# Kernel optimization log

Measured on AMD Instinct MI355X. Metric: run time of the kernel, lower is better.

Reference implementation:

```python
import jax, jax.numpy as jnp
import numpy as np

B, C, D = 1024, 100000, 512
S_SCALE, MARGIN, EPS = 64.0, 0.5, 1e-7  # arcface defaults


def setup_inputs() -> dict:
    key = jax.random.key(0)
    kx, kl, kw = jax.random.split(key, 3)
    x = jax.random.normal(kx, (B, D), dtype=jnp.float32)
    labels = jax.random.randint(kl, (B,), 0, C, dtype=jnp.int64)
    # nn.Linear default init: U(-1/sqrt(fan_in), 1/sqrt(fan_in))
    bound = 1.0 / np.sqrt(D)
    W = jax.random.uniform(kw, (C, D), dtype=jnp.float32, minval=-bound, maxval=bound)
    return {"x": x, "labels": labels, "W": W}


def reference(x, labels, W):
    # L2-normalize features (W is NOT normalized in the original -- the
    # normalize loop there rebinds a local and is a no-op).
    xn = x / jnp.maximum(jnp.linalg.norm(x, axis=1, keepdims=True), 1e-12)
    wf = jnp.einsum('bd,cd->bc', xn, W)               # [B, C] cosine-like logits
    target = jnp.take_along_axis(wf, labels[:, None], axis=1)[:, 0]  # [B]
    # arcface: s * cos(acos(clamp(cos_theta)) + m)
    numerator = S_SCALE * jnp.cos(
        jnp.arccos(jnp.clip(target, -1.0 + EPS, 1.0 - EPS)) + MARGIN)
    # sum over excluded classes = full sum - label term
    excl_sum = jnp.sum(jnp.exp(S_SCALE * wf), axis=1) - jnp.exp(S_SCALE * target)
    L = numerator - jnp.log(jnp.exp(numerator) + excl_sum)
    return -jnp.mean(L)
```

## Files before the change

### kernel.cpp

```cpp
#include <hip/hip_runtime.h>
#include <hip/hip_bf16.h>
#include <math.h>

#define NB 1024
#define NC 100000
#define ND 512
#define SSCALE 64.0f
#define MMARGIN 0.5f

#define BM 128
#define BN 128
#define BK 64
#define NKS (ND / BK)
#define NRT (NB / BM)
#define NCT ((NC + BN - 1) / BN)
#define GRIDSZ (NRT * NCT)

typedef __bf16 bf16x8 __attribute__((ext_vector_type(8)));
typedef float f32x4 __attribute__((ext_vector_type(4)));

__device__ __forceinline__ void gload_lds16(const void* g, void* l) {
    __builtin_amdgcn_global_load_lds(
        (const __attribute__((address_space(1))) unsigned int*)g,
        (__attribute__((address_space(3))) unsigned int*)l, 16, 0, 0);
}


__global__ void prep_kernel(const float* __restrict__ x, __bf16* __restrict__ xnb) {
    const int row = blockIdx.x;
    const int tid = threadIdx.x;
    const float2 v = *reinterpret_cast<const float2*>(x + (size_t)row * ND + tid * 2);
    float ss = v.x * v.x + v.y * v.y;
#pragma unroll
    for (int m = 1; m < 64; m <<= 1) ss += __shfl_xor(ss, m);
    __shared__ float wsum[4];
    if ((tid & 63) == 0) wsum[tid >> 6] = ss;
    __syncthreads();
    const float tot = wsum[0] + wsum[1] + wsum[2] + wsum[3];
    const float inv = 1.0f / fmaxf(sqrtf(tot), 1e-12f);
    __bf16* dst = xnb + (size_t)row * ND + tid * 2;
    dst[0] = (__bf16)(v.x * inv);
    dst[1] = (__bf16)(v.y * inv);
}

__global__ void target_kernel(const __bf16* __restrict__ xnb, const float* __restrict__ Wg,
                              const int* __restrict__ labels, float* __restrict__ tgt) {
    const int wid  = threadIdx.x >> 6;
    const int lane = threadIdx.x & 63;
    const int row  = blockIdx.x * 4 + wid;
    const int lab  = labels[row];
    const int k    = lane * 8;
    const bf16x8 xv = *reinterpret_cast<const bf16x8*>(xnb + (size_t)row * ND + k);
    const float* wr = Wg + (size_t)lab * ND + k;
    const float4 w0 = *reinterpret_cast<const float4*>(wr);
    const float4 w1 = *reinterpret_cast<const float4*>(wr + 4);
    float s = (float)xv[0] * w0.x + (float)xv[1] * w0.y + (float)xv[2] * w0.z + (float)xv[3] * w0.w
            + (float)xv[4] * w1.x + (float)xv[5] * w1.y + (float)xv[6] * w1.z + (float)xv[7] * w1.w;
#pragma unroll
    for (int m = 1; m < 64; m <<= 1) s += __shfl_xor(s, m);
    if (lane == 0) tgt[row] = s;
}

__global__ __launch_bounds__(256, 3) void gemm_exp_kernel(const __bf16* __restrict__ xnb,
                                                          const float* __restrict__ Wg,
                                                          float* __restrict__ sums) {
    __shared__ char lds[49152];
    const int tid  = threadIdx.x;
    const int wid  = tid >> 6;
    const int lane = tid & 63;
    const int l15  = lane & 15;
    const int lhi  = lane >> 4;
    const int wr   = wid >> 1;
    const int wc   = wid & 1;

    const int logical = (blockIdx.x & 7) * (GRIDSZ / 8) + (blockIdx.x >> 3);
    const int rt = logical & 7;
    const int ct = logical >> 3;
    const int r0 = rt * BM;
    const int c0 = ct * BN;

    float4 bw[8];

    const int bcls = (tid >> 3);
    const int bqp  = tid & 7;

    auto loadB = [&](int t) {
#pragma unroll
        for (int l = 0; l < 4; ++l) {
            const int cls = l * 32 + bcls;
            const float* src = Wg + (size_t)(c0 + cls) * ND + t * BK + bqp * 8;
            if (c0 + cls < NC) {
                bw[l * 2]     = *reinterpret_cast<const float4*>(src);
                bw[l * 2 + 1] = *reinterpret_cast<const float4*>(src + 4);
            } else {
                bw[l * 2]     = make_float4(0.f, 0.f, 0.f, 0.f);
                bw[l * 2 + 1] = make_float4(0.f, 0.f, 0.f, 0.f);
            }
        }
    };
    auto writeB = [&]() {
#pragma unroll
        for (int l = 0; l < 4; ++l) {
            const int cls = l * 32 + bcls;
            struct alignas(16) bf8s { __bf16 h[8]; };
            bf8s h;
            const float4 v0 = bw[l * 2], v1 = bw[l * 2 + 1];
            h.h[0] = (__bf16)v0.x; h.h[1] = (__bf16)v0.y; h.h[2] = (__bf16)v0.z; h.h[3] = (__bf16)v0.w;
            h.h[4] = (__bf16)v1.x; h.h[5] = (__bf16)v1.y; h.h[6] = (__bf16)v1.z; h.h[7] = (__bf16)v1.w;
            const int byte = 32768 + cls * 128 + ((bqp ^ (cls & 7)) << 4);
            *reinterpret_cast<bf8s*>(lds + byte) = h;
        }
    };
    auto stageA = [&](int t, int buf) {
#pragma unroll
        for (int it = 0; it < 4; ++it) {
            const int row = it * 32 + wid * 8 + (lane >> 3);
            const int c   = lane & 7;
            const int lc  = c ^ (row & 7);
            const char* src = (const char*)xnb + (size_t)(r0 + row) * (ND * 2) + t * (BK * 2) + lc * 16;
            char* dstbase = lds + buf * 16384 + it * 4096 + wid * 1024;
            gload_lds16(src, dstbase);
        }
    };

    f32x4 acc[4][4] = {};

    auto compute = [&](int buf) {
#pragma unroll
        for (int kk = 0; kk < 2; ++kk) {
            bf16x8 a[4], b[4];
#pragma unroll
            for (int i = 0; i < 4; ++i) {
                const int r = wr * 64 + i * 16 + l15;
                const int byte = buf * 16384 + r * 128 + ((((kk << 2) | lhi) ^ (r & 7)) << 4);
                a[i] = *reinterpret_cast<const bf16x8*>(lds + byte);
            }
#pragma unroll
            for (int j = 0; j < 4; ++j) {
                const int cc = wc * 64 + j * 16 + l15;
                const int byte = 32768 + cc * 128 + ((((kk << 2) | lhi) ^ (cc & 7)) << 4);
                b[j] = *reinterpret_cast<const bf16x8*>(lds + byte);
            }
#pragma unroll
            for (int i = 0; i < 4; ++i)
#pragma unroll
                for (int j = 0; j < 4; ++j)
                    acc[i][j] = __builtin_amdgcn_mfma_f32_16x16x32_bf16(a[i], b[j], acc[i][j], 0, 0, 0);
        }
    };

    loadB(0);
    stageA(0, 0);
    writeB();
    __syncthreads();
    int cur = 0;
#pragma unroll 1
    for (int t = 0; t < NKS; ++t) {
        if (t + 1 < NKS) {
            loadB(t + 1);
            stageA(t + 1, cur ^ 1);
        }
        compute(cur);
        __syncthreads();
        if (t + 1 < NKS) writeB();
        __syncthreads();
        cur ^= 1;
    }

#pragma unroll
    for (int i = 0; i < 4; ++i) {
#pragma unroll
        for (int r = 0; r < 4; ++r) {
            float v = 0.f;
#pragma unroll
            for (int j = 0; j < 4; ++j) {
                const int c = c0 + wc * 64 + j * 16 + l15;
                v += (c < NC) ? __expf(SSCALE * acc[i][j][r]) : 0.f;
            }
            v += __shfl_xor(v, 1);
            v += __shfl_xor(v, 2);
            v += __shfl_xor(v, 4);
            v += __shfl_xor(v, 8);
            if (l15 == 0) {
                const int row = r0 + wr * 64 + i * 16 + lhi * 4 + r;
                atomicAdd(&sums[row], v);
            }
        }
    }
}

__global__ void finalize_kernel(const float* __restrict__ sums, const float* __restrict__ tgt,
                                float* __restrict__ out) {
    const int tid  = threadIdx.x;
    const int wid  = tid >> 6;
    const int lane = tid & 63;
    float t  = tgt[tid];
    const float se = sums[tid];
    t = fminf(fmaxf(t, -1.0f + 1e-7f), 1.0f - 1e-7f);
    const float numer = SSCALE * cosf(acosf(t) + MMARGIN);
    const float excl  = se - expf(SSCALE * t);
    float L = numer - logf(expf(numer) + excl);
#pragma unroll
    for (int m = 1; m < 64; m <<= 1) L += __shfl_xor(L, m);
    __shared__ float ws2[16];
    if (lane == 0) ws2[wid] = L;
    __syncthreads();
    if (tid == 0) {
        float tot = 0.f;
        for (int i = 0; i < 16; ++i) tot += ws2[i];
        out[0] = -(tot / (float)NB);
    }
}

extern "C" void kernel_launch(void* const* d_in, const int* in_sizes, int n_in,
                              void* d_out, int out_size, void* d_ws, size_t ws_size,
                              hipStream_t stream) {
    const float* x      = (const float*)d_in[0];
    const int*   labels = (const int*)d_in[1];
    const float* W      = (const float*)d_in[2];
    float* out = (float*)d_out;

    char* wsb = (char*)d_ws;
    __bf16* xnb  = (__bf16*)wsb;
    float*  sums = (float*)(wsb + (size_t)NB * ND * 2);
    float*  tgt  = sums + NB;

    hipMemsetAsync(sums, 0, NB * sizeof(float), stream);
    prep_kernel<<<NB, 256, 0, stream>>>(x, xnb);
    target_kernel<<<NB / 4, 256, 0, stream>>>(xnb, W, labels, tgt);
    gemm_exp_kernel<<<GRIDSZ, 256, 0, stream>>>(xnb, W, sums);
    finalize_kernel<<<1, 1024, 0, stream>>>(sums, tgt, out);
}
```

Baseline: 194.1 us.

## Pre-convert W to bf16 and stage both GEMM operands via direct global-to-LDS loads

Adds a separate pass that converts W (fp32) to a padded bf16 copy in workspace. The GEMM then stages both A and B tiles with global_load_lds into double-buffered LDS, removing per-block fp32 loads, register conversion and the extra barrier. W is read once at fp32 and once at bf16 instead of being re-read in fp32 by all 8 row tiles. In exchange LDS grows to 64KB, occupancy drops to 2 blocks per CU, and the conversion pass plus workspace space are needed; the old register path remains as a fallback with double-buffered B.

```diff
diff --git a/kernel.cpp b/kernel.cpp
--- a/kernel.cpp
+++ b/kernel.cpp
@@ -15,6 +15,11 @@
 #define NRT (NB / BM)
 #define NCT ((NC + BN - 1) / BN)
 #define GRIDSZ (NRT * NCT)
+#define NCPAD (NCT * BN)
+
+#define ABUF  16384
+#define BBASE 32768
+#define BBUF  16384
 
 typedef __bf16 bf16x8 __attribute__((ext_vector_type(8)));
 typedef float f32x4 __attribute__((ext_vector_type(4)));
@@ -61,10 +66,23 @@
     if (lane == 0) tgt[row] = s;
 }
 
-__global__ __launch_bounds__(256, 3) void gemm_exp_kernel(const __bf16* __restrict__ xnb,
-                                                          const float* __restrict__ Wg,
+__global__ void cvtw_kernel(const float* __restrict__ W, __bf16* __restrict__ Wbf) {
+    const size_t gid = (size_t)blockIdx.x * 256 + threadIdx.x;
+    bf16x8 h = {};
+    if (gid * 8 < (size_t)NC * ND) {
+        const float4 v0 = *reinterpret_cast<const float4*>(W + gid * 8);
+        const float4 v1 = *reinterpret_cast<const float4*>(W + gid * 8 + 4);
+        h[0] = (__bf16)v0.x; h[1] = (__bf16)v0.y; h[2] = (__bf16)v0.z; h[3] = (__bf16)v0.w;
+        h[4] = (__bf16)v1.x; h[5] = (__bf16)v1.y; h[6] = (__bf16)v1.z; h[7] = (__bf16)v1.w;
+    }
+    *reinterpret_cast<bf16x8*>(Wbf + gid * 8) = h;
+}
+
+template<int BMODE>
+__global__ __launch_bounds__(256, 2) void gemm_exp_kernel(const __bf16* __restrict__ xnb,
+                                                          const void* __restrict__ Bsrc,
                                                           float* __restrict__ sums) {
-    __shared__ char lds[49152];
+    __shared__ char lds[65536];
     const int tid  = threadIdx.x;
     const int wid  = tid >> 6;
     const int lane = tid & 63;
@@ -79,16 +97,32 @@
     const int r0 = rt * BM;
     const int c0 = ct * BN;
 
+    auto stageA = [&](int t, int buf) {
+#pragma unroll
+        for (int s = 0; s < 4; ++s) {
+            const int row = s * 32 + wid * 8 + (lane >> 3);
+            const int lc  = (lane & 7) ^ (row & 7);
+            const char* src = (const char*)xnb + (size_t)(r0 + row) * 1024 + t * 128 + lc * 16;
+            gload_lds16(src, lds + buf * ABUF + s * 4096 + wid * 1024);
+        }
+    };
+    auto stageB = [&](int t, int buf) {
+#pragma unroll
+        for (int s = 0; s < 4; ++s) {
+            const int cls = s * 32 + wid * 8 + (lane >> 3);
+            const int lc  = (lane & 7) ^ (cls & 7);
+            const char* src = (const char*)Bsrc + (size_t)(c0 + cls) * 1024 + t * 128 + lc * 16;
+            gload_lds16(src, lds + BBASE + buf * BBUF + s * 4096 + wid * 1024);
+        }
+    };
+    const int bcls = tid >> 3;
+    const int bqp  = tid & 7;
     float4 bw[8];
-
-    const int bcls = (tid >> 3);
-    const int bqp  = tid & 7;
-
     auto loadB = [&](int t) {
 #pragma unroll
         for (int l = 0; l < 4; ++l) {
             const int cls = l * 32 + bcls;
-            const float* src = Wg + (size_t)(c0 + cls) * ND + t * BK + bqp * 8;
+            const float* src = (const float*)Bsrc + (size_t)(c0 + cls) * ND + t * BK + bqp * 8;
             if (c0 + cls < NC) {
                 bw[l * 2]     = *reinterpret_cast<const float4*>(src);
                 bw[l * 2 + 1] = *reinterpret_cast<const float4*>(src + 4);
@@ -98,7 +132,7 @@
             }
         }
     };
-    auto writeB = [&]() {
+    auto writeB = [&](int buf) {
 #pragma unroll
         for (int l = 0; l < 4; ++l) {
             const int cls = l * 32 + bcls;
@@ -107,19 +141,8 @@
             const float4 v0 = bw[l * 2], v1 = bw[l * 2 + 1];
             h.h[0] = (__bf16)v0.x; h.h[1] = (__bf16)v0.y; h.h[2] = (__bf16)v0.z; h.h[3] = (__bf16)v0.w;
             h.h[4] = (__bf16)v1.x; h.h[5] = (__bf16)v1.y; h.h[6] = (__bf16)v1.z; h.h[7] = (__bf16)v1.w;
-            const int byte = 32768 + cls * 128 + ((bqp ^ (cls & 7)) << 4);
+            const int byte = BBASE + buf * BBUF + cls * 128 + ((bqp ^ (cls & 7)) << 4);
             *reinterpret_cast<bf8s*>(lds + byte) = h;
-        }
-    };
-    auto stageA = [&](int t, int buf) {
-#pragma unroll
-        for (int it = 0; it < 4; ++it) {
-            const int row = it * 32 + wid * 8 + (lane >> 3);
-            const int c   = lane & 7;
-            const int lc  = c ^ (row & 7);
-            const char* src = (const char*)xnb + (size_t)(r0 + row) * (ND * 2) + t * (BK * 2) + lc * 16;
-            char* dstbase = lds + buf * 16384 + it * 4096 + wid * 1024;
-            gload_lds16(src, dstbase);
         }
     };
 
@@ -129,17 +152,18 @@
 #pragma unroll
         for (int kk = 0; kk < 2; ++kk) {
             bf16x8 a[4], b[4];
+            const int ck = (kk << 2) | lhi;
 #pragma unroll
             for (int i = 0; i < 4; ++i) {
                 const int r = wr * 64 + i * 16 + l15;
-                const int byte = buf * 16384 + r * 128 + ((((kk << 2) | lhi) ^ (r & 7)) << 4);
-                a[i] = *reinterpret_cast<const bf16x8*>(lds + byte);
+                a[i] = *reinterpret_cast<const bf16x8*>(
+                    lds + buf * ABUF + r * 128 + ((ck ^ (r & 7)) << 4));
             }
 #pragma unroll
             for (int j = 0; j < 4; ++j) {
-                const int cc = wc * 64 + j * 16 + l15;
-                const int byte = 32768 + cc * 128 + ((((kk << 2) | lhi) ^ (cc & 7)) << 4);
-                b[j] = *reinterpret_cast<const bf16x8*>(lds + byte);
+                const int cls = wc * 64 + j * 16 + l15;
+                b[j] = *reinterpret_cast<const bf16x8*>(
+                    lds + BBASE + buf * BBUF + cls * 128 + ((ck ^ (cls & 7)) << 4));
             }
 #pragma unroll
             for (int i = 0; i < 4; ++i)
@@ -149,22 +173,37 @@
         }
     };
 
-    loadB(0);
-    stageA(0, 0);
-    writeB();
-    __syncthreads();
-    int cur = 0;
+    if constexpr (BMODE == 0) {
+        stageA(0, 0);
+        stageB(0, 0);
+        __syncthreads();
 #pragma unroll 1
-    for (int t = 0; t < NKS; ++t) {
-        if (t + 1 < NKS) {
-            loadB(t + 1);
-            stageA(t + 1, cur ^ 1);
-        }
-        compute(cur);
+        for (int t = 0; t < NKS; ++t) {
+            const int buf = t & 1;
+            if (t + 1 < NKS) {
+                stageA(t + 1, buf ^ 1);
+                stageB(t + 1, buf ^ 1);
+            }
+            compute(buf);
+            __syncthreads();
+        }
+    } else {
+        loadB(0);
+        stageA(0, 0);
+        loadB(1);
+        writeB(0);
         __syncthreads();
-        if (t + 1 < NKS) writeB();
-        __syncthreads();
-        cur ^= 1;
+#pragma unroll 1
+        for (int t = 0; t < NKS; ++t) {
+            const int buf = t & 1;
+            if (t + 1 < NKS) {
+                stageA(t + 1, buf ^ 1);
+                loadB(t + 1);
+            }
+            compute(buf);
+            if (t + 1 < NKS) writeB(buf ^ 1);
+            __syncthreads();
+        }
     }
 
 #pragma unroll
@@ -222,12 +261,19 @@
 
     char* wsb = (char*)d_ws;
     __bf16* xnb  = (__bf16*)wsb;
-    float*  sums = (float*)(wsb + (size_t)NB * ND * 2);
-    float*  tgt  = sums + NB;
+    float*  sums = (float*)(wsb + 1048576);
+    float*  tgt  = (float*)(wsb + 1052672);
+    __bf16* Wbf  = (__bf16*)(wsb + 1056768);
+    const size_t WS_NEED = 1056768ull + (size_t)NCPAD * ND * 2;
 
     hipMemsetAsync(sums, 0, NB * sizeof(float), stream);
     prep_kernel<<<NB, 256, 0, stream>>>(x, xnb);
     target_kernel<<<NB / 4, 256, 0, stream>>>(xnb, W, labels, tgt);
-    gemm_exp_kernel<<<GRIDSZ, 256, 0, stream>>>(xnb, W, sums);
+    if (ws_size >= WS_NEED) {
+        cvtw_kernel<<<((size_t)NCPAD * ND) / (256 * 8), 256, 0, stream>>>(W, Wbf);
+        gemm_exp_kernel<0><<<GRIDSZ, 256, 0, stream>>>(xnb, Wbf, sums);
+    } else {
+        gemm_exp_kernel<1><<<GRIDSZ, 256, 0, stream>>>(xnb, W, sums);
+    }
     finalize_kernel<<<1, 1024, 0, stream>>>(sums, tgt, out);
 }
```

After: 240.6 us. 24.0% more time.
